# Optimization experiments

Hardware: AMD Instinct MI355X
Metric: run time of the kernel (lower is better)

The kernel has to match this reference:

```python
import jax, jax.numpy as jnp
import numpy as np

B, N, T, D = 8, 64, 256, 80          # batch, hidden states, mel frames, frame_channels
E, P, H, O = 512, 256, 512, 512      # encoder_dim, prenet_dim, memory_rnn_dim, outputnet hidden
STD_FLOOR = 1e-3
EPS = 1e-4                            # OverflowUtils.log_clamped eps
NEG_INF = -1e6                        # finite stand-in for -inf: exp underflows to 0, grads stay finite
LOG2PI = float(np.log(2.0 * np.pi))


def _log_clamped(x):
    return jnp.log(jnp.maximum(x, EPS))


def setup_inputs() -> dict:
    ks = jax.random.split(jax.random.key(0), 12)
    s = 0.02
    return {
        "inputs": jax.random.normal(ks[0], (B, N, E), jnp.float32),
        "mels": jax.random.normal(ks[1], (B, D, T), jnp.float32),
        "prenet_w1": jax.random.normal(ks[2], (P, D), jnp.float32) * s,
        "prenet_w2": jax.random.normal(ks[3], (P, P), jnp.float32) * s,
        "w_ih": jax.random.normal(ks[4], (4 * H, P), jnp.float32) * s,
        "w_hh": jax.random.normal(ks[5], (4 * H, H), jnp.float32) * s,
        "b_ih": jnp.zeros((4 * H,), jnp.float32),
        "b_hh": jnp.zeros((4 * H,), jnp.float32),
        "out_w1": jax.random.normal(ks[6], (O, H + E), jnp.float32) * s,
        "out_b1": jnp.zeros((O,), jnp.float32),
        "out_w2": jax.random.normal(ks[7], (2 * D + 1, O), jnp.float32) * s,
        "out_b2": jnp.zeros((2 * D + 1,), jnp.float32),
        "inputs_len": jax.random.randint(ks[8], (B,), N // 2, N + 1),
        "mel_lens": jax.random.randint(ks[9], (B,), T // 2, T + 1),
    }


def _forward(inputs, mels, prenet_w1, prenet_w2, w_ih, w_hh, b_ih, b_hh,
             out_w1, out_b1, out_w2, out_b2, inputs_len, mel_lens):
    mels_btd = jnp.swapaxes(mels, 1, 2)  # (B,T,D)
    # _add_go_token with ar_order=1: shift right by one frame, zero go token
    ar_inputs = jnp.concatenate([jnp.zeros_like(mels_btd[:, :1]), mels_btd[:, :-1]], axis=1)
    state_mask = jnp.arange(N)[None, :] < inputs_len[:, None]       # (B,N)
    log_priors = jnp.where(jnp.arange(N) == 0, 0.0, NEG_INF)        # left-to-right start in state 0

    def step(carry, xs):
        h, c, prev_alpha = carry
        ar_t, x_t, t = xs
        # Prenet (bias-free Linear + ReLU, dropout disabled)
        p = jax.nn.relu(ar_t @ prenet_w1.T)
        p = jax.nn.relu(p @ prenet_w2.T)
        # LSTMCell (torch gate order i,f,g,o)
        gates = p @ w_ih.T + b_ih + h @ w_hh.T + b_hh
        i, f, g, o = jnp.split(gates, 4, axis=-1)
        c_new = jax.nn.sigmoid(f) * c + jax.nn.sigmoid(i) * jnp.tanh(g)
        h_new = jax.nn.sigmoid(o) * jnp.tanh(c_new)
        # Outputnet: broadcast memory over states, concat with encoder outputs, MLP
        z = jnp.concatenate([jnp.broadcast_to(h_new[:, None, :], (B, N, H)), inputs], axis=-1)
        hid = jax.nn.relu(jnp.einsum("bnf,of->bno", z, out_w1) + out_b1)
        params = jnp.einsum("bno,po->bnp", hid, out_w2) + out_b2     # (B,N,2D+1)
        mean = params[..., :D]
        std = jnp.maximum(jax.nn.softplus(params[..., D:2 * D]), STD_FLOOR)
        trans_vec = params[..., 2 * D]                               # (B,N)
        # EmissionModel: Normal log_prob summed over features, state-masked
        lp = -0.5 * jnp.square((x_t[:, None, :] - mean) / std) - jnp.log(std) - 0.5 * LOG2PI
        emission = jnp.sum(lp, axis=-1) * state_mask                 # (B,N)
        # TransitionModel: stay/leave in log domain
        staying = prev_alpha + _log_clamped(jax.nn.sigmoid(-trans_vec))
        leaving = jnp.roll(prev_alpha + _log_clamped(jax.nn.sigmoid(trans_vec)), 1, axis=1)
        leaving = leaving.at[:, 0].set(NEG_INF)
        trans_term = jnp.where(state_mask, jnp.logaddexp(staying, leaving), NEG_INF)
        alpha_temp = jnp.where(t == 0, log_priors[None, :] + emission, emission + trans_term)
        log_c_t = jax.nn.logsumexp(alpha_temp, axis=1)               # (B,)
        alpha = alpha_temp - log_c_t[:, None]
        return (h_new, c_new, alpha), (log_c_t, alpha, trans_vec)

    carry0 = (jnp.zeros((B, H), mels.dtype), jnp.zeros((B, H), mels.dtype),
              jnp.zeros((B, N), mels.dtype))
    xs = (jnp.swapaxes(ar_inputs, 0, 1), jnp.swapaxes(mels_btd, 0, 1), jnp.arange(T))
    _, (log_c, log_alpha, trans_mat) = jax.lax.scan(step, carry0, xs)
    log_c = jnp.swapaxes(log_c, 0, 1)           # (B,T)
    log_alpha = jnp.swapaxes(log_alpha, 0, 1)   # (B,T,N)
    trans_mat = jnp.swapaxes(trans_mat, 0, 1)   # (B,T,N)
    # _mask_lengths + sum of per-step scaling factors
    t_mask = jnp.arange(T)[None, :] < mel_lens[:, None]
    sum_log_c = jnp.sum(log_c * t_mask, axis=1)
    # absorption-state scaling factor at t = mel_lens-1, transitioning out of state inputs_len-1
    idx = jnp.broadcast_to((mel_lens - 1)[:, None, None], (B, 1, N))
    last_alpha = jnp.take_along_axis(log_alpha, idx, axis=1)[:, 0]   # (B,N)
    last_alpha = jnp.where(state_mask, last_alpha, NEG_INF)
    last_tv = jnp.take_along_axis(trans_mat, idx, axis=1)[:, 0]
    last_state = jnp.arange(N)[None, :] == (inputs_len - 1)[:, None]
    log_trans_p = jnp.where(last_state, _log_clamped(jax.nn.sigmoid(last_tv)), NEG_INF)
    sum_final_log_c = jax.nn.logsumexp(last_alpha + log_trans_p, axis=1)
    return sum_log_c + sum_final_log_c           # (B,) sequence log-likelihood


def reference(inputs, mels, prenet_w1, prenet_w2, w_ih, w_hh, b_ih, b_hh,
              out_w1, out_b1, out_w2, out_b2, inputs_len, mel_lens):
    return _forward(inputs, mels, prenet_w1, prenet_w2, w_ih, w_hh, b_ih, b_hh,
                    out_w1, out_b1, out_w2, out_b2, inputs_len, mel_lens)
```

## Files before the change

### kernel.cpp

```cpp
#include <hip/hip_runtime.h>
#include <math.h>

#define T_STEPS 256
#define BB 8
#define NSTATE 64
#define DD 80
#define PP 256
#define HH 512
#define OO 512
#define NPARAM 161
#define PLS 171
#define NEG_INF_F (-1000000.0f)

#define GSTR 88

typedef __attribute__((ext_vector_type(8))) short s16x8;
typedef __attribute__((ext_vector_type(4))) float f32x4;
typedef _Float16 h2t __attribute__((ext_vector_type(2)));

union PairU { double d; float f[2]; unsigned u[2]; };

__device__ __forceinline__ float sigmoidf_(float x) { return 1.0f / (1.0f + __expf(-x)); }
__device__ __forceinline__ unsigned short bf16rne(float x) {
  union { float f; unsigned u; } v; v.f = x;
  unsigned r = (v.u + 0x7FFFu + ((v.u >> 16) & 1u)) >> 16;
  return (unsigned short)r;
}
__device__ __forceinline__ float bf2f(unsigned s) {
  union { unsigned u; float f; } v; v.u = s << 16; return v.f;
}
__device__ __forceinline__ float fdot2_(unsigned a, unsigned b, float c) {
  union { unsigned u; h2t h; } ua, ub; ua.u = a; ub.u = b;
  return __builtin_amdgcn_fdot2(ua.h, ub.h, c, false);
}
__device__ __forceinline__ unsigned packf16(float a, float b) {
  union { unsigned u; _Float16 f[2]; } p;
  p.f[0] = (_Float16)a; p.f[1] = (_Float16)b;
  return p.u;
}

__global__ __launch_bounds__(256)
void conv_all(const float* __restrict__ w_ih, const float* __restrict__ out_w1,
              const float* __restrict__ inputs, const float* __restrict__ pw2,
              const float* __restrict__ pw1, const float* __restrict__ w2,
              const float* __restrict__ w_hh, const float* __restrict__ mels,
              unsigned short* __restrict__ w_ihb, unsigned* __restrict__ w1h16T,
              unsigned short* __restrict__ w1eb, unsigned short* __restrict__ inputsb,
              unsigned short* __restrict__ w2b, unsigned short* __restrict__ w1b,
              unsigned short* __restrict__ w2frag, unsigned* __restrict__ whh16,
              float* __restrict__ hmfullf, unsigned short* __restrict__ arb)
{
  int idx = blockIdx.x * 256 + threadIdx.x;
  if (idx < 524288) {
    w_ihb[idx] = bf16rne(w_ih[idx]);
  } else if (idx < 655360) {
    int i = idx - 524288; int pp = i >> 9, o = i & 511;
    w1h16T[i] = packf16(out_w1[(size_t)o * 1024 + 2 * pp],
                        out_w1[(size_t)o * 1024 + 2 * pp + 1]);
  } else if (idx < 917504) {
    int i = idx - 655360; int r = i >> 9, c = i & 511;
    w1eb[i] = bf16rne(out_w1[(size_t)r * 1024 + 512 + c]);
  } else if (idx < 1179648) {
    int i = idx - 917504;
    inputsb[i] = bf16rne(inputs[i]);
  } else if (idx < 1245184) {
    int i = idx - 1179648;
    w2b[i] = bf16rne(pw2[i]);
  } else if (idx < 1277952) {
    int i = idx - 1245184; int r = i >> 7, c = i & 127;
    w1b[i] = (c < DD) ? bf16rne(pw1[r * DD + c]) : (unsigned short)0;
  } else if (idx < 1376256) {
    int i = idx - 1277952;
    int j = i & 7, lane = (i >> 3) & 63, nt = (i >> 9) % 12, kb = i / 6144;
    int p = nt * 16 + (lane & 15);
    int o = kb * 32 + ((lane >> 4) << 3) + j;
    float v = (p < NPARAM) ? w2[p * OO + o] : 0.0f;
    w2frag[i] = bf16rne(v);
  } else if (idx < 1900544) {
    int i = idx - 1376256;
    int gr = i >> 8, pp = i & 255;
    const float* src = &w_hh[(size_t)gr * HH + pp * 2];
    whh16[i] = packf16(src[0], src[1]);
  } else if (idx < 2949120) {
    hmfullf[idx - 1900544] = 0.0f;
  } else if (idx < 3211264) {
    int i = idx - 2949120;
    int c = i & 127; int r = i >> 7; int b = r & 7; int t = r >> 3;
    float v = (t == 0 || c >= DD) ? 0.0f : mels[(b * DD + c) * T_STEPS + (t - 1)];
    arb[i] = bf16rne(v);
  }
}

__device__ __forceinline__
void gemm_tile(const unsigned short* __restrict__ A, int lda,
               const unsigned short* __restrict__ B, int ldb,
               const float* __restrict__ bias1, const float* __restrict__ bias2,
               void* __restrict__ Cout, int N, int K, int relu, int obf,
               int m0, int n0, unsigned short* As, unsigned short* Bs)
{
  const int tid = threadIdx.x;
  const int lane = tid & 63, wv = tid >> 6;
  const int srow = tid >> 3, scol = (tid & 7) * 8;

  f32x4 acc[4];
#pragma unroll
  for (int m = 0; m < 4; ++m) acc[m] = (f32x4){0.f, 0.f, 0.f, 0.f};

  for (int k0 = 0; k0 < K; k0 += 64) {
    __syncthreads();
    *(float4*)&As[srow * GSTR + scol] =
        *(const float4*)&A[(size_t)(m0 + srow) * lda + k0 + scol];
    *(float4*)&As[(srow + 32) * GSTR + scol] =
        *(const float4*)&A[(size_t)(m0 + srow + 32) * lda + k0 + scol];
    *(float4*)&Bs[srow * GSTR + scol] =
        *(const float4*)&B[(size_t)(n0 + srow) * ldb + k0 + scol];
    *(float4*)&Bs[(srow + 32) * GSTR + scol] =
        *(const float4*)&B[(size_t)(n0 + srow + 32) * ldb + k0 + scol];
    __syncthreads();
#pragma unroll
    for (int ks = 0; ks < 2; ++ks) {
      const int kk = ks * 32 + 8 * (lane >> 4);
      s16x8 bfr = *(const s16x8*)&Bs[(wv * 16 + (lane & 15)) * GSTR + kk];
#pragma unroll
      for (int m = 0; m < 4; ++m) {
        s16x8 afr = *(const s16x8*)&As[(m * 16 + (lane & 15)) * GSTR + kk];
        acc[m] = __builtin_amdgcn_mfma_f32_16x16x32_bf16(afr, bfr, acc[m], 0, 0, 0);
      }
    }
  }
  const int cn = n0 + wv * 16 + (lane & 15);
  float bj = 0.f;
  if (bias1) bj += bias1[cn];
  if (bias2) bj += bias2[cn];
  const int rbase = m0 + (lane >> 4) * 4;
#pragma unroll
  for (int m = 0; m < 4; ++m)
#pragma unroll
    for (int r = 0; r < 4; ++r) {
      float v = acc[m][r] + bj;
      if (relu) v = fmaxf(v, 0.f);
      size_t ci = (size_t)(rbase + m * 16 + r) * N + cn;
      if (obf) ((unsigned short*)Cout)[ci] = bf16rne(v);
      else     ((float*)Cout)[ci] = v;
    }
}

__global__ __launch_bounds__(256)
void gemm_mfma(const unsigned short* __restrict__ A, int lda,
               const unsigned short* __restrict__ B, int ldb,
               const float* __restrict__ bias1, const float* __restrict__ bias2,
               void* __restrict__ Cout, int N, int K, int relu, int obf)
{
  __shared__ unsigned short As[64 * GSTR];
  __shared__ unsigned short Bs[64 * GSTR];
  gemm_tile(A, lda, B, ldb, bias1, bias2, Cout, N, K, relu, obf,
            blockIdx.y * 64, blockIdx.x * 64, As, Bs);
}

__global__ __launch_bounds__(256)
void gemm_pair(const unsigned short* __restrict__ p2b, const unsigned short* __restrict__ w_ihb,
               const float* __restrict__ b_ih, const float* __restrict__ b_hh,
               unsigned short* __restrict__ gatesb,
               const unsigned short* __restrict__ inputsb, const unsigned short* __restrict__ w1eb,
               const float* __restrict__ out_b1, float* __restrict__ zi)
{
  __shared__ unsigned short As[64 * GSTR];
  __shared__ unsigned short Bs[64 * GSTR];
  int bid = blockIdx.x;
  if (bid < 1024) {
    gemm_tile(p2b, 256, w_ihb, 256, b_ih, b_hh, gatesb, 2048, 256, 0, 1,
              (bid >> 5) * 64, (bid & 31) * 64, As, Bs);
  } else {
    int i = bid - 1024;
    gemm_tile(inputsb, 512, w1eb, 512, out_b1, nullptr, zi, 512, 512, 0, 0,
              (i >> 3) * 64, (i & 7) * 64, As, Bs);
  }
}

__global__ __launch_bounds__(512)
void mega(const unsigned* __restrict__ whh16, const unsigned short* __restrict__ gatesb,
          const unsigned* __restrict__ w1h16T, const float* __restrict__ zi,
          const unsigned short* __restrict__ w2frag, const float* __restrict__ b2,
          const float* __restrict__ mels, const int* __restrict__ inputs_len,
          double* __restrict__ hmfull, float* __restrict__ elp)
{
  const int tid = threadIdx.x;

  if (blockIdx.x < 128) {
    __shared__ unsigned hl16[256];
    __shared__ float red[4][128];
    const int b = blockIdx.x & 7;
    const int s = blockIdx.x >> 3;
    const int j0 = s * 32;
    const int row = tid & 127;
    const int kq  = tid >> 7;
    const int g = row >> 5, jl = row & 31;
    const int gr = g * HH + j0 + jl;

    unsigned wreg[64];
    {
      const unsigned* wp = &whh16[(size_t)gr * 256 + kq * 64];
#pragma unroll
      for (int c = 0; c < 64; ++c) wreg[c] = wp[c];
    }
    float c_reg = 0.f;

    for (int t = 0; t < T_STEPS; ++t) {
      float gxv[4] = {0.f, 0.f, 0.f, 0.f};
      if (tid < 32) {
        const unsigned short* gp = &gatesb[((size_t)t * BB + b) * 2048 + j0 + tid];
#pragma unroll
        for (int gg = 0; gg < 4; ++gg) gxv[gg] = bf2f(gp[gg * HH]);
      }

      if (t == 0) {
        if (tid < 256) hl16[tid] = 0u;
      } else if (tid < 256) {
        const double* src = hmfull + ((size_t)(t - 1) * BB + b) * 256;
        PairU w;
        for (;;) {
          w.d = __hip_atomic_load(&src[tid], __ATOMIC_RELAXED, __HIP_MEMORY_SCOPE_AGENT);
          if (w.u[1] == (unsigned)t) break;
          __builtin_amdgcn_s_sleep(1);
        }
        hl16[tid] = w.u[0];
      }
      __syncthreads();

      float a0 = 0.f, a1 = 0.f, a2 = 0.f, a3 = 0.f;
      const unsigned* hp = &hl16[kq * 64];
#pragma unroll
      for (int c = 0; c < 64; c += 4) {
        a0 = fdot2_(wreg[c + 0], hp[c + 0], a0);
        a1 = fdot2_(wreg[c + 1], hp[c + 1], a1);
        a2 = fdot2_(wreg[c + 2], hp[c + 2], a2);
        a3 = fdot2_(wreg[c + 3], hp[c + 3], a3);
      }
      red[kq][row] = (a0 + a1) + (a2 + a3);
      __syncthreads();

      if (tid < 32) {
        float iv = red[0][tid]       + red[1][tid]       + red[2][tid]       + red[3][tid]       + gxv[0];
        float fv = red[0][32 + tid]  + red[1][32 + tid]  + red[2][32 + tid]  + red[3][32 + tid]  + gxv[1];
        float gv = red[0][64 + tid]  + red[1][64 + tid]  + red[2][64 + tid]  + red[3][64 + tid]  + gxv[2];
        float ov = red[0][96 + tid]  + red[1][96 + tid]  + red[2][96 + tid]  + red[3][96 + tid]  + gxv[3];
        float ct = sigmoidf_(fv) * c_reg + sigmoidf_(iv) * tanhf(gv);
        c_reg = ct;
        float h = sigmoidf_(ov) * tanhf(ct);
        float hpart = __shfl_xor(h, 1);
        if ((tid & 1) == 0) {
          PairU pv;
          pv.u[0] = packf16(h, hpart);
          pv.u[1] = (unsigned)(t + 1);
          __hip_atomic_store(&hmfull[((size_t)t * BB + b) * 256 + s * 16 + (tid >> 1)],
                             pv.d, __ATOMIC_RELAXED, __HIP_MEMORY_SCOPE_AGENT);
        }
      }
    }
    return;
  }

  __shared__ unsigned hl16w[256];
  __shared__ float hvs[OO];
  __shared__ float xts[96];
  __shared__ s16x8 Afr[2][256];
  __shared__ float pl[64 * PLS];

  const int wb = blockIdx.x - 128;

  for (int it = 0; it < 8; ++it) {
    const int item = wb + (it << 8);
    const int t = item >> 3, bb = item & 7;
    const double* src = hmfull + ((size_t)t * BB + bb) * 256;

    if (tid < 16) {
      for (;;) {
        PairU w;
        w.d = __hip_atomic_load(&src[tid * 16], __ATOMIC_RELAXED, __HIP_MEMORY_SCOPE_AGENT);
        if (__all(w.u[1] == (unsigned)(t + 1))) break;
        __builtin_amdgcn_s_sleep(1);
      }
    }
    __syncthreads();
    if (tid < 256) {
      PairU w;
      for (;;) {
        w.d = __hip_atomic_load(&src[tid], __ATOMIC_RELAXED, __HIP_MEMORY_SCOPE_AGENT);
        if (w.u[1] == (unsigned)(t + 1)) break;
        __builtin_amdgcn_s_sleep(1);
      }
      hl16w[tid] = w.u[0];
    } else if (tid - 256 < DD) {
      xts[tid - 256] = mels[(bb * DD + (tid - 256)) * T_STEPS + t];
    }
    __syncthreads();

    {
      float a0 = 0.f, a1 = 0.f, a2 = 0.f, a3 = 0.f;
#pragma unroll 8
      for (int c = 0; c < 256; c += 4) {
        a0 = fdot2_(w1h16T[(size_t)(c + 0) * 512 + tid], hl16w[c + 0], a0);
        a1 = fdot2_(w1h16T[(size_t)(c + 1) * 512 + tid], hl16w[c + 1], a1);
        a2 = fdot2_(w1h16T[(size_t)(c + 2) * 512 + tid], hl16w[c + 2], a2);
        a3 = fdot2_(w1h16T[(size_t)(c + 3) * 512 + tid], hl16w[c + 3], a3);
      }
      hvs[tid] = (a0 + a1) + (a2 + a3);
    }
    __syncthreads();

    const int lane = tid & 63, wv = (tid >> 6) & 3;
    const int n_state = wv * 16 + (lane & 15);
    const int osub = (lane >> 4) * 8;
    const float* zbase = zi + (size_t)(bb * 64 + n_state) * OO;

    auto genA = [&](int kb, int buf) {
      int ob = kb * 32 + osub;
      float4 z0 = *(const float4*)&zbase[ob];
      float4 z1 = *(const float4*)&zbase[ob + 4];
      float4 h0 = *(const float4*)&hvs[ob];
      float4 h1 = *(const float4*)&hvs[ob + 4];
      s16x8 s;
      s[0] = bf16rne(fmaxf(z0.x + h0.x, 0.f));
      s[1] = bf16rne(fmaxf(z0.y + h0.y, 0.f));
      s[2] = bf16rne(fmaxf(z0.z + h0.z, 0.f));
      s[3] = bf16rne(fmaxf(z0.w + h0.w, 0.f));
      s[4] = bf16rne(fmaxf(z1.x + h1.x, 0.f));
      s[5] = bf16rne(fmaxf(z1.y + h1.y, 0.f));
      s[6] = bf16rne(fmaxf(z1.z + h1.z, 0.f));
      s[7] = bf16rne(fmaxf(z1.w + h1.w, 0.f));
      Afr[buf][tid] = s;
    };

    f32x4 acc[4][3];
#pragma unroll
    for (int m = 0; m < 4; ++m)
#pragma unroll
      for (int n = 0; n < 3; ++n) acc[m][n] = (f32x4){0.f, 0.f, 0.f, 0.f};

    if (tid < 256) genA(0, 0);

    for (int kb = 0; kb < 16; ++kb) {
      __syncthreads();
      if (tid < 256) {
        const unsigned short* bfp = w2frag + ((size_t)(wv * 3) * 64 + lane) * 8;
        s16x8 bf[3];
#pragma unroll
        for (int ntl = 0; ntl < 3; ++ntl)
          bf[ntl] = *(const s16x8*)&bfp[(size_t)kb * 6144 + ntl * 512];
        if (kb < 15) genA(kb + 1, (kb + 1) & 1);
        s16x8 af[4];
#pragma unroll
        for (int m = 0; m < 4; ++m) af[m] = Afr[kb & 1][m * 64 + lane];
#pragma unroll
        for (int m = 0; m < 4; ++m)
#pragma unroll
          for (int ntl = 0; ntl < 3; ++ntl)
            acc[m][ntl] = __builtin_amdgcn_mfma_f32_16x16x32_bf16(af[m], bf[ntl], acc[m][ntl], 0, 0, 0);
      }
    }

    if (tid < 256) {
      const int prow4 = (lane >> 4) * 4;
#pragma unroll
      for (int ntl = 0; ntl < 3; ++ntl) {
        int p = (wv * 3 + ntl) * 16 + (lane & 15);
        if (p < NPARAM) {
          float bb2 = b2[p];
#pragma unroll
          for (int m = 0; m < 4; ++m)
#pragma unroll
            for (int r = 0; r < 4; ++r)
              pl[(m * 16 + prow4 + r) * PLS + p] = acc[m][ntl][r] + bb2;
        }
      }
    }
    __syncthreads();

    if (tid < 256) {
      const int ne = tid >> 2, dq = tid & 3;
      float s = 0.f;
      for (int d = dq * 20; d < dq * 20 + 20; ++d) {
        float mean = pl[ne * PLS + d];
        float sp   = pl[ne * PLS + 80 + d];
        float x = xts[d];
        float sf = (sp > 20.f) ? sp : log1pf(__expf(sp));
        float sd = fmaxf(sf, 0.001f);
        float zz = (x - mean) / sd;
        s += -0.5f * zz * zz - __logf(sd) - 0.91893853320467274f;
      }
      s += __shfl_xor(s, 1);
      s += __shfl_xor(s, 2);
      if (dq == 0) {
        int ilen = inputs_len[bb];
        float tv = pl[ne * PLS + 160];
        float4 o;
        o.x = (ne < ilen) ? s : 0.f;
        o.y = __logf(fmaxf(sigmoidf_(-tv), 1e-4f));
        o.z = __logf(fmaxf(sigmoidf_(tv), 1e-4f));
        o.w = 0.f;
        *(float4*)&elp[((size_t)item * NSTATE + ne) * 4] = o;
      }
    }
    __syncthreads();
  }
}

__global__ __launch_bounds__(64)
void hmm_scan(const float* __restrict__ elp, const int* __restrict__ inputs_len,
              const int* __restrict__ mel_lens, float* __restrict__ out)
{
  const int b = blockIdx.x;
  const int n = threadIdx.x;
  const int ilen = inputs_len[b], mlen = mel_lens[b];
  const bool mask = n < ilen;
  const float4* e4 = (const float4*)elp;
  const size_t base = (size_t)b * NSTATE + n;
  float beta = 0.f, la = NEG_INF_F, llsp = 0.f;
  float4 cur = e4[base];

  for (int t = 0; t < T_STEPS; ++t) {
    float4 nxt = {0.f, 0.f, 0.f, 0.f};
    if (t + 1 < T_STEPS) nxt = e4[base + (size_t)(t + 1) * BB * NSTATE];
    float e = cur.x, ln_ = cur.y, lp_ = cur.z;
    if (t == 0) {
      beta = ((n == 0) ? 0.f : NEG_INF_F) + e;
    } else {
      float stay = beta + ln_;
      float lvs = beta + lp_;
      float lv = __shfl_up(lvs, 1, 64);
      if (n == 0) lv = NEG_INF_F;
      float mx = fmaxf(stay, lv), mn = fminf(stay, lv);
      float tt = mask ? (mx + log1pf(__expf(mn - mx))) : NEG_INF_F;
      beta = e + tt;
    }
    if (t == mlen - 1) { la = mask ? beta : NEG_INF_F; llsp = lp_; }
    cur = nxt;
  }

  float v = la + ((n == ilen - 1) ? llsp : NEG_INF_F);
  float m = v;
#pragma unroll
  for (int off = 1; off < 64; off <<= 1) m = fmaxf(m, __shfl_xor(m, off));
  float es = __expf(v - m);
#pragma unroll
  for (int off = 1; off < 64; off <<= 1) es += __shfl_xor(es, off);
  if (n == 0) out[b] = m + __logf(es);
}

extern "C" void kernel_launch(void* const* d_in, const int* in_sizes, int n_in,
                              void* d_out, int out_size, void* d_ws, size_t ws_size,
                              hipStream_t stream)
{
  const float* inputs    = (const float*)d_in[0];
  const float* mels      = (const float*)d_in[1];
  const float* prenet_w1 = (const float*)d_in[2];
  const float* prenet_w2 = (const float*)d_in[3];
  const float* w_ih      = (const float*)d_in[4];
  const float* w_hh      = (const float*)d_in[5];
  const float* b_ih      = (const float*)d_in[6];
  const float* b_hh      = (const float*)d_in[7];
  const float* out_w1    = (const float*)d_in[8];
  const float* out_b1    = (const float*)d_in[9];
  const float* out_w2    = (const float*)d_in[10];
  const float* out_b2    = (const float*)d_in[11];
  const int* inputs_len  = (const int*)d_in[12];
  const int* mel_lens    = (const int*)d_in[13];

  float* ws = (float*)d_ws;
  unsigned short* gatesb  = (unsigned short*)ws;
  float* zi      = ws + 2097152;
  float* elp     = ws + 2359296;
  double* hmfull = (double*)(ws + 2883584);
  unsigned short* w2frag  = (unsigned short*)(ws + 3932160);
  unsigned short* p2b     = (unsigned short*)(ws + 3981312);
  unsigned short* p1b     = (unsigned short*)(ws + 4243456);
  unsigned short* arb     = (unsigned short*)(ws + 4505600);
  unsigned short* w1b     = (unsigned short*)(ws + 4636672);
  unsigned short* w2b     = (unsigned short*)(ws + 4653056);
  unsigned short* w_ihb   = (unsigned short*)(ws + 4685824);
  unsigned short* w1eb    = (unsigned short*)(ws + 4947968);
  unsigned short* inputsb = (unsigned short*)(ws + 5079040);
  unsigned* whh16         = (unsigned*)(ws + 5210112);
  unsigned* w1h16T        = (unsigned*)(ws + 5734400);

  conv_all<<<12544, 256, 0, stream>>>(w_ih, out_w1, inputs, prenet_w2, prenet_w1,
                                      out_w2, w_hh, mels, w_ihb, w1h16T, w1eb,
                                      inputsb, w2b, w1b, w2frag, whh16,
                                      (float*)hmfull, arb);

  gemm_mfma<<<dim3(4, 32), 256, 0, stream>>>(arb, 128, w1b, 128,
                                             nullptr, nullptr, p1b, PP, 128, 1, 1);
  gemm_mfma<<<dim3(4, 32), 256, 0, stream>>>(p1b, 256, w2b, 256,
                                             nullptr, nullptr, p2b, PP, 256, 1, 1);
  gemm_pair<<<1088, 256, 0, stream>>>(p2b, w_ihb, b_ih, b_hh, gatesb,
                                      inputsb, w1eb, out_b1, zi);

  mega<<<384, 512, 0, stream>>>(whh16, gatesb, w1h16T, zi, w2frag, out_b2,
                                mels, inputs_len, hmfull, elp);

  hmm_scan<<<8, 64, 0, stream>>>(elp, inputs_len, mel_lens, (float*)d_out);
}
```

Baseline: 554.7 us.

## Fuse HMM forward scan into mega kernel as flag-polling consumer block

Removes the separate hmm_scan launch and adds a 385th block to the mega kernel that runs the HMM forward recursion, polling per-timestep emission records as producer blocks publish them. Emission and transition values are packed into one 64-bit atomic word (fp32 emission plus two bf16 log-transition terms, whose sign bits double as the ready flag), so the scan overlaps the output-net work. The zeroing of hmfull moves from conv_all into a hipMemsetAsync that also clears the new elpP buffer. The costs are bf16 rounding of the log-transition terms and a reliance on all 385 blocks being co-resident so the spinning consumer cannot deadlock.

```diff
diff --git a/kernel.cpp b/kernel.cpp
--- a/kernel.cpp
+++ b/kernel.cpp
@@ -48,7 +48,7 @@
               unsigned short* __restrict__ w1eb, unsigned short* __restrict__ inputsb,
               unsigned short* __restrict__ w2b, unsigned short* __restrict__ w1b,
               unsigned short* __restrict__ w2frag, unsigned* __restrict__ whh16,
-              float* __restrict__ hmfullf, unsigned short* __restrict__ arb)
+              unsigned short* __restrict__ arb)
 {
   int idx = blockIdx.x * 256 + threadIdx.x;
   if (idx < 524288) {
@@ -81,10 +81,8 @@
     int gr = i >> 8, pp = i & 255;
     const float* src = &w_hh[(size_t)gr * HH + pp * 2];
     whh16[i] = packf16(src[0], src[1]);
-  } else if (idx < 2949120) {
-    hmfullf[idx - 1900544] = 0.0f;
-  } else if (idx < 3211264) {
-    int i = idx - 2949120;
+  } else if (idx < 2162688) {
+    int i = idx - 1900544;
     int c = i & 127; int r = i >> 7; int b = r & 7; int t = r >> 3;
     float v = (t == 0 || c >= DD) ? 0.0f : mels[(b * DD + c) * T_STEPS + (t - 1)];
     arb[i] = bf16rne(v);
@@ -182,7 +180,9 @@
           const unsigned* __restrict__ w1h16T, const float* __restrict__ zi,
           const unsigned short* __restrict__ w2frag, const float* __restrict__ b2,
           const float* __restrict__ mels, const int* __restrict__ inputs_len,
-          double* __restrict__ hmfull, float* __restrict__ elp)
+          const int* __restrict__ mel_lens,
+          double* __restrict__ hmfull, double* __restrict__ elpP,
+          float* __restrict__ outp)
 {
   const int tid = threadIdx.x;
 
@@ -257,6 +257,48 @@
         }
       }
     }
+    return;
+  }
+
+  if (blockIdx.x == 384) {
+    const int b = tid >> 6, n = tid & 63;
+    const int ilen = inputs_len[b], mlen = mel_lens[b];
+    const bool mask = n < ilen;
+    float beta = 0.f, la = NEG_INF_F, llsp = 0.f;
+
+    for (int t = 0; t < T_STEPS; ++t) {
+      PairU w;
+      const double* src = &elpP[((size_t)t * BB + b) * NSTATE + n];
+      for (;;) {
+        w.d = __hip_atomic_load(src, __ATOMIC_RELAXED, __HIP_MEMORY_SCOPE_AGENT);
+        if ((w.u[1] & 0x80008000u) == 0x80008000u) break;
+        __builtin_amdgcn_s_sleep(1);
+      }
+      float e   = w.f[0];
+      float ln_ = bf2f(w.u[1] & 0xFFFFu);
+      float lp_ = bf2f(w.u[1] >> 16);
+      if (t == 0) {
+        beta = ((n == 0) ? 0.f : NEG_INF_F) + e;
+      } else {
+        float stay = beta + ln_;
+        float lvs = beta + lp_;
+        float lv = __shfl_up(lvs, 1, 64);
+        if (n == 0) lv = NEG_INF_F;
+        float mx = fmaxf(stay, lv), mn = fminf(stay, lv);
+        float tt = mask ? (mx + log1pf(__expf(mn - mx))) : NEG_INF_F;
+        beta = e + tt;
+      }
+      if (t == mlen - 1) { la = mask ? beta : NEG_INF_F; llsp = lp_; }
+    }
+
+    float v = la + ((n == ilen - 1) ? llsp : NEG_INF_F);
+    float m = v;
+#pragma unroll
+    for (int off = 1; off < 64; off <<= 1) m = fmaxf(m, __shfl_xor(m, off));
+    float es = __expf(v - m);
+#pragma unroll
+    for (int off = 1; off < 64; off <<= 1) es += __shfl_xor(es, off);
+    if (n == 0) outp[b] = m + __logf(es);
     return;
   }
 
@@ -393,58 +435,17 @@
       if (dq == 0) {
         int ilen = inputs_len[bb];
         float tv = pl[ne * PLS + 160];
-        float4 o;
-        o.x = (ne < ilen) ? s : 0.f;
-        o.y = __logf(fmaxf(sigmoidf_(-tv), 1e-4f));
-        o.z = __logf(fmaxf(sigmoidf_(tv), 1e-4f));
-        o.w = 0.f;
-        *(float4*)&elp[((size_t)item * NSTATE + ne) * 4] = o;
+        float lsn_ = __logf(fmaxf(sigmoidf_(-tv), 1e-4f));
+        float lsp_ = __logf(fmaxf(sigmoidf_(tv), 1e-4f));
+        PairU pv;
+        pv.f[0] = (ne < ilen) ? s : 0.f;
+        pv.u[1] = (unsigned)bf16rne(lsn_) | ((unsigned)bf16rne(lsp_) << 16);
+        __hip_atomic_store(&elpP[((size_t)item) * NSTATE + ne], pv.d,
+                           __ATOMIC_RELAXED, __HIP_MEMORY_SCOPE_AGENT);
       }
     }
     __syncthreads();
   }
-}
-
-__global__ __launch_bounds__(64)
-void hmm_scan(const float* __restrict__ elp, const int* __restrict__ inputs_len,
-              const int* __restrict__ mel_lens, float* __restrict__ out)
-{
-  const int b = blockIdx.x;
-  const int n = threadIdx.x;
-  const int ilen = inputs_len[b], mlen = mel_lens[b];
-  const bool mask = n < ilen;
-  const float4* e4 = (const float4*)elp;
-  const size_t base = (size_t)b * NSTATE + n;
-  float beta = 0.f, la = NEG_INF_F, llsp = 0.f;
-  float4 cur = e4[base];
-
-  for (int t = 0; t < T_STEPS; ++t) {
-    float4 nxt = {0.f, 0.f, 0.f, 0.f};
-    if (t + 1 < T_STEPS) nxt = e4[base + (size_t)(t + 1) * BB * NSTATE];
-    float e = cur.x, ln_ = cur.y, lp_ = cur.z;
-    if (t == 0) {
-      beta = ((n == 0) ? 0.f : NEG_INF_F) + e;
-    } else {
-      float stay = beta + ln_;
-      float lvs = beta + lp_;
-      float lv = __shfl_up(lvs, 1, 64);
-      if (n == 0) lv = NEG_INF_F;
-      float mx = fmaxf(stay, lv), mn = fminf(stay, lv);
-      float tt = mask ? (mx + log1pf(__expf(mn - mx))) : NEG_INF_F;
-      beta = e + tt;
-    }
-    if (t == mlen - 1) { la = mask ? beta : NEG_INF_F; llsp = lp_; }
-    cur = nxt;
-  }
-
-  float v = la + ((n == ilen - 1) ? llsp : NEG_INF_F);
-  float m = v;
-#pragma unroll
-  for (int off = 1; off < 64; off <<= 1) m = fmaxf(m, __shfl_xor(m, off));
-  float es = __expf(v - m);
-#pragma unroll
-  for (int off = 1; off < 64; off <<= 1) es += __shfl_xor(es, off);
-  if (n == 0) out[b] = m + __logf(es);
 }
 
 extern "C" void kernel_launch(void* const* d_in, const int* in_sizes, int n_in,
@@ -469,24 +470,25 @@
   float* ws = (float*)d_ws;
   unsigned short* gatesb  = (unsigned short*)ws;
   float* zi      = ws + 2097152;
-  float* elp     = ws + 2359296;
-  double* hmfull = (double*)(ws + 2883584);
-  unsigned short* w2frag  = (unsigned short*)(ws + 3932160);
-  unsigned short* p2b     = (unsigned short*)(ws + 3981312);
-  unsigned short* p1b     = (unsigned short*)(ws + 4243456);
-  unsigned short* arb     = (unsigned short*)(ws + 4505600);
-  unsigned short* w1b     = (unsigned short*)(ws + 4636672);
-  unsigned short* w2b     = (unsigned short*)(ws + 4653056);
-  unsigned short* w_ihb   = (unsigned short*)(ws + 4685824);
-  unsigned short* w1eb    = (unsigned short*)(ws + 4947968);
-  unsigned short* inputsb = (unsigned short*)(ws + 5079040);
-  unsigned* whh16         = (unsigned*)(ws + 5210112);
-  unsigned* w1h16T        = (unsigned*)(ws + 5734400);
-
-  conv_all<<<12544, 256, 0, stream>>>(w_ih, out_w1, inputs, prenet_w2, prenet_w1,
-                                      out_w2, w_hh, mels, w_ihb, w1h16T, w1eb,
-                                      inputsb, w2b, w1b, w2frag, whh16,
-                                      (float*)hmfull, arb);
+  double* hmfull = (double*)(ws + 2359296);
+  double* elpP   = (double*)(ws + 3407872);
+  unsigned short* w2frag  = (unsigned short*)(ws + 3670016);
+  unsigned short* p2b     = (unsigned short*)(ws + 3719168);
+  unsigned short* p1b     = (unsigned short*)(ws + 3981312);
+  unsigned short* arb     = (unsigned short*)(ws + 4243456);
+  unsigned short* w1b     = (unsigned short*)(ws + 4374528);
+  unsigned short* w2b     = (unsigned short*)(ws + 4390912);
+  unsigned short* w_ihb   = (unsigned short*)(ws + 4423680);
+  unsigned short* w1eb    = (unsigned short*)(ws + 4685824);
+  unsigned short* inputsb = (unsigned short*)(ws + 4816896);
+  unsigned* whh16         = (unsigned*)(ws + 4947968);
+  unsigned* w1h16T        = (unsigned*)(ws + 5472256);
+
+  hipMemsetAsync((void*)hmfull, 0, 5242880, stream);
+
+  conv_all<<<8448, 256, 0, stream>>>(w_ih, out_w1, inputs, prenet_w2, prenet_w1,
+                                     out_w2, w_hh, mels, w_ihb, w1h16T, w1eb,
+                                     inputsb, w2b, w1b, w2frag, whh16, arb);
 
   gemm_mfma<<<dim3(4, 32), 256, 0, stream>>>(arb, 128, w1b, 128,
                                              nullptr, nullptr, p1b, PP, 128, 1, 1);
@@ -495,8 +497,7 @@
   gemm_pair<<<1088, 256, 0, stream>>>(p2b, w_ihb, b_ih, b_hh, gatesb,
                                       inputsb, w1eb, out_b1, zi);
 
-  mega<<<384, 512, 0, stream>>>(whh16, gatesb, w1h16T, zi, w2frag, out_b2,
-                                mels, inputs_len, hmfull, elp);
-
-  hmm_scan<<<8, 64, 0, stream>>>(elp, inputs_len, mel_lens, (float*)d_out);
-}
+  mega<<<385, 512, 0, stream>>>(whh16, gatesb, w1h16T, zi, w2frag, out_b2,
+                                mels, inputs_len, mel_lens, hmfull, elpP,
+                                (float*)d_out);
+}
```

Result: faster. 475.4 us (-14.3%).
